# Kernel optimization log

Measured on AMD Instinct MI355X. Metric: run time of the kernel, lower is better.

Reference implementation:

```python
import math
import jax, jax.numpy as jnp
import numpy as np

B, T, E = 1, 4096, 768
H, D = 12, 64
RA_WINDOW = 512
INIT_GATES = (2.2, 0.6, 0.1)


def setup_inputs() -> dict:
    key = jax.random.key(0)
    ks = jax.random.split(key, 6)
    x = jax.random.normal(ks[0], (B, T, E), dtype=jnp.float32)
    # Linear weights stored as [in, out] (math-equivalent to torch's x @ W.T)
    s = 1.0 / math.sqrt(E)
    Wq = jax.random.normal(ks[1], (E, H * D), dtype=jnp.float32) * s
    Wk = jax.random.normal(ks[2], (E, H * D), dtype=jnp.float32) * s
    Wv = jax.random.normal(ks[3], (E, H * D), dtype=jnp.float32) * s
    Wo = jax.random.normal(ks[4], (H * D, E), dtype=jnp.float32) * s
    gates = jnp.tile(jnp.asarray(INIT_GATES, dtype=jnp.float32)[None, :], (H, 1))  # [H,3]
    u = jax.random.normal(ks[5], (H, D), dtype=jnp.float32) * 0.02
    return {"x": x, "Wq": Wq, "Wk": Wk, "Wv": Wv, "Wo": Wo, "gates": gates, "u": u}


def reference(x, Wq, Wk, Wv, Wo, gates, u):
    # projections -> [B,H,T,D]
    def proj(W):
        return (x @ W).reshape(B, T, H, D).transpose(0, 2, 1, 3)
    Q, K, V = proj(Wq), proj(Wk), proj(Wv)

    S = jnp.einsum('bhtd,bhsd->bhts', Q, K) / math.sqrt(D)  # [B,H,T,T]

    w = jax.nn.softmax(gates, axis=-1)  # [H,3]
    w_std = w[:, 0][None, :, None, None]
    w_rec = w[:, 1][None, :, None, None]
    w_disc = w[:, 2][None, :, None, None]

    logits = w_std * S + w_rec * jnp.swapaxes(S, -2, -1)

    # discoverability column bias from K via per-head u
    d_raw = jnp.einsum('bhtd,hd->bht', K, u)
    d = d_raw - jnp.mean(d_raw, axis=-1, keepdims=True)
    logits = logits + w_disc * d[:, :, None, :]

    # causal banded mask
    idx = jnp.arange(T)
    mask = (idx[None, :] <= idx[:, None]) & (jnp.abs(idx[None, :] - idx[:, None]) <= RA_WINDOW)
    logits = jnp.where(mask[None, None, :, :], logits, -jnp.inf)

    attn = jax.nn.softmax(logits, axis=-1)
    ctx = jnp.einsum('bhts,bhsd->bhtd', attn, V)
    out = ctx.transpose(0, 2, 1, 3).reshape(B, T, H * D) @ Wo
    return (out, attn)
```

## Files before the change

### kernel.cpp

```cpp
#include <hip/hip_runtime.h>
#include <cstddef>

#define T_LEN 4096
#define EMB 768
#define NH 12
#define HD 64
#define WIN 512

#define GBM 128
#define GBN 128
#define GBK 16

__global__ __launch_bounds__(256) void gemm3_f32(const float* __restrict__ A,
                                                 const float* __restrict__ B0,
                                                 const float* __restrict__ B1,
                                                 const float* __restrict__ B2,
                                                 float* __restrict__ C0,
                                                 float* __restrict__ C1,
                                                 float* __restrict__ C2,
                                                 int M, int N, int K) {
    __shared__ float As[GBK][GBM + 4];
    __shared__ float Bs[GBK][GBN + 4];
    const int tid = threadIdx.x;
    const int bm = blockIdx.y * GBM;
    const int bn = blockIdx.x * GBN;
    const float* __restrict__ B = (blockIdx.z == 0) ? B0 : (blockIdx.z == 1) ? B1 : B2;
    float* __restrict__ C = (blockIdx.z == 0) ? C0 : (blockIdx.z == 1) ? C1 : C2;

    const int ty = (tid >> 4) << 2;
    const int tx = (tid & 15) << 2;

    const int ar = tid >> 1;
    const int ac = (tid & 1) << 3;
    const int br = tid >> 4;
    const int bc = (tid & 15) << 3;

    float acc[8][8] = {};

    float4 pa0 = *(const float4*)&A[(size_t)(bm + ar) * K + ac];
    float4 pa1 = *(const float4*)&A[(size_t)(bm + ar) * K + ac + 4];
    float4 pb0 = *(const float4*)&B[(size_t)br * N + bn + bc];
    float4 pb1 = *(const float4*)&B[(size_t)br * N + bn + bc + 4];

    for (int k0 = 0; k0 < K; k0 += GBK) {
        As[ac + 0][ar] = pa0.x; As[ac + 1][ar] = pa0.y; As[ac + 2][ar] = pa0.z; As[ac + 3][ar] = pa0.w;
        As[ac + 4][ar] = pa1.x; As[ac + 5][ar] = pa1.y; As[ac + 6][ar] = pa1.z; As[ac + 7][ar] = pa1.w;
        *(float4*)&Bs[br][bc]     = pb0;
        *(float4*)&Bs[br][bc + 4] = pb1;
        __syncthreads();
        if (k0 + GBK < K) {
            pa0 = *(const float4*)&A[(size_t)(bm + ar) * K + k0 + GBK + ac];
            pa1 = *(const float4*)&A[(size_t)(bm + ar) * K + k0 + GBK + ac + 4];
            pb0 = *(const float4*)&B[(size_t)(k0 + GBK + br) * N + bn + bc];
            pb1 = *(const float4*)&B[(size_t)(k0 + GBK + br) * N + bn + bc + 4];
        }
#pragma unroll
        for (int k = 0; k < GBK; ++k) {
            const float4 a0v = *(const float4*)&As[k][ty];
            const float4 a1v = *(const float4*)&As[k][ty + 64];
            const float4 b0v = *(const float4*)&Bs[k][tx];
            const float4 b1v = *(const float4*)&Bs[k][tx + 64];
            const float av[8] = {a0v.x, a0v.y, a0v.z, a0v.w, a1v.x, a1v.y, a1v.z, a1v.w};
            const float bv[8] = {b0v.x, b0v.y, b0v.z, b0v.w, b1v.x, b1v.y, b1v.z, b1v.w};
#pragma unroll
            for (int i = 0; i < 8; ++i)
#pragma unroll
                for (int j = 0; j < 8; ++j)
                    acc[i][j] += av[i] * bv[j];
        }
        __syncthreads();
    }
#pragma unroll
    for (int i = 0; i < 8; ++i) {
        const int r = bm + ty + ((i < 4) ? i : (60 + i));
        *(float4*)&C[(size_t)r * N + bn + tx]      = make_float4(acc[i][0], acc[i][1], acc[i][2], acc[i][3]);
        *(float4*)&C[(size_t)r * N + bn + tx + 64] = make_float4(acc[i][4], acc[i][5], acc[i][6], acc[i][7]);
    }
}

__global__ __launch_bounds__(256) void dbias_kernel(const float* __restrict__ K,
                                                    const float* __restrict__ u,
                                                    float* __restrict__ d_bias) {
    const int h = blockIdx.x;
    const int tid = threadIdx.x;
    __shared__ __align__(16) float us[HD];
    __shared__ float dr[T_LEN];
    __shared__ float red[256];
    if (tid < HD) us[tid] = u[h * HD + tid];
    __syncthreads();
    const float4* u4 = (const float4*)us;
    float lsum = 0.f;
    for (int t = tid; t < T_LEN; t += 256) {
        const float4* Kp = (const float4*)&K[(size_t)t * EMB + h * HD];
        float acc = 0.f;
#pragma unroll
        for (int i = 0; i < HD / 4; ++i) {
            float4 k4 = Kp[i];
            float4 uu = u4[i];
            acc += k4.x * uu.x + k4.y * uu.y + k4.z * uu.z + k4.w * uu.w;
        }
        dr[t] = acc;
        lsum += acc;
    }
    red[tid] = lsum;
    __syncthreads();
    for (int off = 128; off > 0; off >>= 1) {
        if (tid < off) red[tid] += red[tid + off];
        __syncthreads();
    }
    const float mean = red[0] * (1.0f / (float)T_LEN);
    __syncthreads();
    for (int t = tid; t < T_LEN; t += 256) {
        d_bias[h * T_LEN + t] = dr[t] - mean;
    }
}

__global__ __launch_bounds__(256) void attn_band_kernel(const float* __restrict__ Q,
                                                        const float* __restrict__ K,
                                                        const float* __restrict__ V,
                                                        const float* __restrict__ d_bias,
                                                        const float* __restrict__ gates,
                                                        float* __restrict__ attn,
                                                        float* __restrict__ ctx) {
    const int t0  = blockIdx.x << 6;
    const int h   = blockIdx.y;
    const int tid = threadIdx.x;
    const int cg  = tid & 15;
    const int tm  = (tid >> 4) << 2;
    const int tn4 = cg << 2;

    const int lm = tid >> 2;
    const int lk = (tid & 3) << 4;
    const int sr = tid >> 1;
    const int sc = (tid & 1) << 5;

    __shared__ __align__(16) float QT[64][68];
    __shared__ __align__(16) float KT[64][68];
    __shared__ __align__(16) float Bc[64][136];
    __shared__ float cmf[5][64];
    __shared__ float rmf[64], idvf[64];
    float* __restrict__ Bp = &Bc[0][0];

    const float g0 = gates[h * 3 + 0];
    const float g1 = gates[h * 3 + 1];
    const float g2 = gates[h * 3 + 2];
    const float gm = fmaxf(g0, fmaxf(g1, g2));
    const float e0 = __expf(g0 - gm), e1 = __expf(g1 - gm), e2 = __expf(g2 - gm);
    const float gi = 1.0f / (e0 + e1 + e2);
    const float w_std = e0 * gi * 0.125f;
    const float w_rec = e1 * gi * 0.125f;
    const float w_disc = e2 * gi;

    const int cp_start = (t0 >= 576) ? 0 : ((576 - t0) >> 7);
    int s0 = t0 - 576 + (cp_start << 7);

    float4 kr[8], qr[8];
    {
        int srow = s0 + sr; srow = srow < 0 ? 0 : srow;
        const float* Kp = K + (size_t)srow * EMB + h * HD + sc;
#pragma unroll
        for (int c = 0; c < 8; ++c) kr[c] = *(const float4*)(Kp + 4 * c);
    }

    {
        const float* Qp = Q + (size_t)(t0 + lm) * EMB + h * HD + lk;
        const float* Kp = K + (size_t)(t0 + lm) * EMB + h * HD + lk;
#pragma unroll
        for (int it = 0; it < 4; ++it) {
            float4 a = *(const float4*)(Qp + 4 * it);
            QT[lk + 4 * it + 0][lm] = a.x;
            QT[lk + 4 * it + 1][lm] = a.y;
            QT[lk + 4 * it + 2][lm] = a.z;
            QT[lk + 4 * it + 3][lm] = a.w;
            float4 b = *(const float4*)(Kp + 4 * it);
            KT[lk + 4 * it + 0][lm] = b.x;
            KT[lk + 4 * it + 1][lm] = b.y;
            KT[lk + 4 * it + 2][lm] = b.z;
            KT[lk + 4 * it + 3][lm] = b.w;
        }
    }

    float rm[4], rden[4], acc[4][4];
#pragma unroll
    for (int i = 0; i < 4; ++i) {
        rm[i] = -1e30f;
        rden[i] = 0.f;
#pragma unroll
        for (int j = 0; j < 4; ++j) acc[i][j] = 0.f;
    }

    for (int cp = cp_start; cp < 5; ++cp) {
        __syncthreads();
#pragma unroll
        for (int c = 0; c < 8; ++c) {
            Bc[sc + 4 * c + 0][sr] = kr[c].x;
            Bc[sc + 4 * c + 1][sr] = kr[c].y;
            Bc[sc + 4 * c + 2][sr] = kr[c].z;
            Bc[sc + 4 * c + 3][sr] = kr[c].w;
        }
        __syncthreads();

        {
            int srow = s0 + sr; srow = srow < 0 ? 0 : srow;
            const float* Qp = Q + (size_t)srow * EMB + h * HD + sc;
#pragma unroll
            for (int c = 0; c < 8; ++c) qr[c] = *(const float4*)(Qp + 4 * c);
        }

        float m1[4][8] = {};
#pragma unroll 8
        for (int k = 0; k < 64; ++k) {
            const float4 a4 = *(const float4*)&QT[k][tm];
            const float4 b0 = *(const float4*)&Bc[k][tn4];
            const float4 b1 = *(const float4*)&Bc[k][tn4 + 64];
            const float av[4] = {a4.x, a4.y, a4.z, a4.w};
            const float bv[8] = {b0.x, b0.y, b0.z, b0.w, b1.x, b1.y, b1.z, b1.w};
#pragma unroll
            for (int i = 0; i < 4; ++i)
#pragma unroll
                for (int j = 0; j < 8; ++j)
                    m1[i][j] += av[i] * bv[j];
        }
        __syncthreads();

#pragma unroll
        for (int c = 0; c < 8; ++c) {
            Bc[sc + 4 * c + 0][sr] = qr[c].x;
            Bc[sc + 4 * c + 1][sr] = qr[c].y;
            Bc[sc + 4 * c + 2][sr] = qr[c].z;
            Bc[sc + 4 * c + 3][sr] = qr[c].w;
        }
        __syncthreads();

        if (cp < 4) {
            int srow = s0 + 128 + sr; srow = srow < 0 ? 0 : srow;
            const float* Kp = K + (size_t)srow * EMB + h * HD + sc;
#pragma unroll
            for (int c = 0; c < 8; ++c) kr[c] = *(const float4*)(Kp + 4 * c);
        }

        float m2[4][8] = {};
#pragma unroll 8
        for (int k = 0; k < 64; ++k) {
            const float4 a4 = *(const float4*)&KT[k][tm];
            const float4 b0 = *(const float4*)&Bc[k][tn4];
            const float4 b1 = *(const float4*)&Bc[k][tn4 + 64];
            const float av[4] = {a4.x, a4.y, a4.z, a4.w};
            const float bv[8] = {b0.x, b0.y, b0.z, b0.w, b1.x, b1.y, b1.z, b1.w};
#pragma unroll
            for (int i = 0; i < 4; ++i)
#pragma unroll
                for (int j = 0; j < 8; ++j)
                    m2[i][j] += av[i] * bv[j];
        }

        const int i0 = s0 + tn4;
        const int i0c = i0 < 0 ? 0 : i0;
        const float4 db0 = *(const float4*)&d_bias[h * T_LEN + i0c];
        const float4 db1 = *(const float4*)&d_bias[h * T_LEN + s0 + 64 + tn4];
        const float dbv[8] = {db0.x, db0.y, db0.z, db0.w, db1.x, db1.y, db1.z, db1.w};
        float l[4][8];
#pragma unroll
        for (int i = 0; i < 4; ++i) {
            const int t = t0 + tm + i;
#pragma unroll
            for (int j = 0; j < 8; ++j) {
                const int s = s0 + ((j < 4) ? (tn4 + j) : (tn4 + j + 60));
                const float lv = w_std * m1[i][j] + w_rec * m2[i][j] + w_disc * dbv[j];
                const bool valid = (s >= 0) && (s <= t) && (s >= t - WIN);
                l[i][j] = valid ? lv : -1e30f;
            }
        }
#pragma unroll
        for (int i = 0; i < 4; ++i) {
            float cmx = fmaxf(fmaxf(fmaxf(l[i][0], l[i][1]), fmaxf(l[i][2], l[i][3])),
                              fmaxf(fmaxf(l[i][4], l[i][5]), fmaxf(l[i][6], l[i][7])));
#pragma unroll
            for (int off = 1; off < 16; off <<= 1) cmx = fmaxf(cmx, __shfl_xor(cmx, off));
            const float nm = fmaxf(rm[i], cmx);
            const float f = __expf(rm[i] - nm);
            float cs = 0.f;
#pragma unroll
            for (int j = 0; j < 8; ++j) {
                const float p = __expf(l[i][j] - nm);
                l[i][j] = p;
                cs += p;
            }
#pragma unroll
            for (int off = 1; off < 16; off <<= 1) cs += __shfl_xor(cs, off);
            rden[i] = rden[i] * f + cs;
            rm[i] = nm;
#pragma unroll
            for (int j = 0; j < 4; ++j) acc[i][j] *= f;
            if (cg == 0) cmf[cp][tm + i] = nm;
            float* arow = &attn[((size_t)(h * T_LEN + t0 + tm + i)) * T_LEN];
            if (s0 >= 0)
                *(float4*)&arow[s0 + tn4] = make_float4(l[i][0], l[i][1], l[i][2], l[i][3]);
            *(float4*)&arow[s0 + 64 + tn4] = make_float4(l[i][4], l[i][5], l[i][6], l[i][7]);
        }
        __syncthreads();

#pragma unroll
        for (int j = 0; j < 4; ++j) {
            *(float4*)&Bp[(tn4 + j) * 68 + tm] =
                make_float4(l[0][j], l[1][j], l[2][j], l[3][j]);
            *(float4*)&Bp[(tn4 + j + 64) * 68 + tm] =
                make_float4(l[0][j + 4], l[1][j + 4], l[2][j + 4], l[3][j + 4]);
        }
        __syncthreads();

#pragma unroll 8
        for (int k = 0; k < 128; ++k) {
            const float4 av = *(const float4*)&Bp[k * 68 + tm];
            int vrow = s0 + k; vrow = vrow < 0 ? 0 : vrow;
            const float4 bv = *(const float4*)&V[(size_t)vrow * EMB + h * HD + tn4];
            acc[0][0] += av.x * bv.x; acc[0][1] += av.x * bv.y; acc[0][2] += av.x * bv.z; acc[0][3] += av.x * bv.w;
            acc[1][0] += av.y * bv.x; acc[1][1] += av.y * bv.y; acc[1][2] += av.y * bv.z; acc[1][3] += av.y * bv.w;
            acc[2][0] += av.z * bv.x; acc[2][1] += av.z * bv.y; acc[2][2] += av.z * bv.z; acc[2][3] += av.z * bv.w;
            acc[3][0] += av.w * bv.x; acc[3][1] += av.w * bv.y; acc[3][2] += av.w * bv.z; acc[3][3] += av.w * bv.w;
        }
        s0 += 128;
    }

    float idv[4];
#pragma unroll
    for (int i = 0; i < 4; ++i) {
        idv[i] = 1.0f / rden[i];
        *(float4*)&ctx[(size_t)(t0 + tm + i) * EMB + h * HD + tn4] =
            make_float4(acc[i][0] * idv[i], acc[i][1] * idv[i], acc[i][2] * idv[i], acc[i][3] * idv[i]);
    }
    if (cg == 0) {
#pragma unroll
        for (int i = 0; i < 4; ++i) {
            rmf[tm + i] = rm[i];
            idvf[tm + i] = idv[i];
        }
    }
    __syncthreads();
    for (int idx = tid; idx < 320; idx += 256) {
        const int c = idx >> 6, r = idx & 63;
        if (c >= cp_start) cmf[c][r] = __expf(cmf[c][r] - rmf[r]) * idvf[r];
    }
    __syncthreads();
    int ss = t0 - 576 + (cp_start << 7);
    for (int cp = cp_start; cp < 5; ++cp, ss += 128) {
#pragma unroll
        for (int half = 0; half < 2; ++half) {
            const int cbase = ss + (half << 6);
            if (cbase >= 0) {
#pragma unroll
                for (int i = 0; i < 4; ++i) {
                    const float f = cmf[cp][tm + i];
                    float* p = &attn[((size_t)(h * T_LEN + t0 + tm + i)) * T_LEN + cbase + tn4];
                    const float4 v = *(const float4*)p;
                    *(float4*)p = make_float4(v.x * f, v.y * f, v.z * f, v.w * f);
                }
            }
        }
    }
    const int sl = t0 - 576 + (cp_start << 7);
    const int stored_left = sl < 0 ? 0 : sl;
    const int wv = tid >> 6, ln = tid & 63;
    const float4 z4 = make_float4(0.f, 0.f, 0.f, 0.f);
    for (int r = wv; r < 64; r += 4) {
        float* arow = attn + ((size_t)(h * T_LEN + t0 + r)) * T_LEN;
        for (int col = ln << 2; col < stored_left; col += 256)
            *(float4*)&arow[col] = z4;
        for (int col = t0 + 64 + (ln << 2); col < T_LEN; col += 256)
            *(float4*)&arow[col] = z4;
    }
}

extern "C" void kernel_launch(void* const* d_in, const int* in_sizes, int n_in,
                              void* d_out, int out_size, void* d_ws, size_t ws_size,
                              hipStream_t stream) {
    const float* x     = (const float*)d_in[0];
    const float* Wq    = (const float*)d_in[1];
    const float* Wk    = (const float*)d_in[2];
    const float* Wv    = (const float*)d_in[3];
    const float* Wo    = (const float*)d_in[4];
    const float* gates = (const float*)d_in[5];
    const float* u     = (const float*)d_in[6];

    float* out  = (float*)d_out;
    float* attn = out + (size_t)T_LEN * EMB;

    float* ws = (float*)d_ws;
    float* Qb = ws;
    float* Kb = Qb + (size_t)T_LEN * EMB;
    float* Vb = Kb + (size_t)T_LEN * EMB;
    float* Cb = Vb + (size_t)T_LEN * EMB;
    float* Db = Cb + (size_t)T_LEN * EMB;

    gemm3_f32<<<dim3(EMB / GBN, T_LEN / GBM, 3), 256, 0, stream>>>(
        x, Wq, Wk, Wv, Qb, Kb, Vb, T_LEN, EMB, EMB);
    dbias_kernel<<<NH, 256, 0, stream>>>(Kb, u, Db);

    attn_band_kernel<<<dim3(T_LEN / 64, NH), 256, 0, stream>>>(Qb, Kb, Vb, Db, gates,
                                                               attn, Cb);

    gemm3_f32<<<dim3(EMB / GBN, T_LEN / GBM, 1), 256, 0, stream>>>(
        Cb, Wo, Wo, Wo, out, out, out, T_LEN, EMB, EMB);
}
```

Before: 1.496 ms.

## Stage band probabilities in compact buffer and expand attn in separate kernel

The attention kernel now writes unnormalized band probabilities into a compact per-row workspace of 640 columns plus five per-chunk rescale factors, instead of writing into the full attn matrix, re-reading it to rescale, and zero-filling. A new expand kernel writes every attn row once, scaling band values and emitting zeros elsewhere in a single coalesced pass. This removes the read-modify-write over the attn output and the scattered zero stores from the compute kernel. In exchange it adds a large workspace, an extra kernel launch, and an extra write and read of the compact buffer.

After: 1.448 ms. 3.2% less time.

```diff
diff --git a/kernel.cpp b/kernel.cpp
--- a/kernel.cpp
+++ b/kernel.cpp
@@ -6,6 +6,7 @@
 #define NH 12
 #define HD 64
 #define WIN 512
+#define PBW 640
 
 #define GBM 128
 #define GBN 128
@@ -120,7 +121,8 @@
                                                         const float* __restrict__ V,
                                                         const float* __restrict__ d_bias,
                                                         const float* __restrict__ gates,
-                                                        float* __restrict__ attn,
+                                                        float* __restrict__ Pb,
+                                                        float* __restrict__ Fb,
                                                         float* __restrict__ ctx) {
     const int t0  = blockIdx.x << 6;
     const int h   = blockIdx.y;
@@ -293,10 +295,9 @@
 #pragma unroll
             for (int j = 0; j < 4; ++j) acc[i][j] *= f;
             if (cg == 0) cmf[cp][tm + i] = nm;
-            float* arow = &attn[((size_t)(h * T_LEN + t0 + tm + i)) * T_LEN];
-            if (s0 >= 0)
-                *(float4*)&arow[s0 + tn4] = make_float4(l[i][0], l[i][1], l[i][2], l[i][3]);
-            *(float4*)&arow[s0 + 64 + tn4] = make_float4(l[i][4], l[i][5], l[i][6], l[i][7]);
+            float* prow = &Pb[((size_t)(h * T_LEN + t0 + tm + i)) * PBW + (cp << 7)];
+            *(float4*)&prow[tn4]      = make_float4(l[i][0], l[i][1], l[i][2], l[i][3]);
+            *(float4*)&prow[64 + tn4] = make_float4(l[i][4], l[i][5], l[i][6], l[i][7]);
         }
         __syncthreads();
 
@@ -339,35 +340,32 @@
     __syncthreads();
     for (int idx = tid; idx < 320; idx += 256) {
         const int c = idx >> 6, r = idx & 63;
-        if (c >= cp_start) cmf[c][r] = __expf(cmf[c][r] - rmf[r]) * idvf[r];
-    }
-    __syncthreads();
-    int ss = t0 - 576 + (cp_start << 7);
-    for (int cp = cp_start; cp < 5; ++cp, ss += 128) {
-#pragma unroll
-        for (int half = 0; half < 2; ++half) {
-            const int cbase = ss + (half << 6);
-            if (cbase >= 0) {
-#pragma unroll
-                for (int i = 0; i < 4; ++i) {
-                    const float f = cmf[cp][tm + i];
-                    float* p = &attn[((size_t)(h * T_LEN + t0 + tm + i)) * T_LEN + cbase + tn4];
-                    const float4 v = *(const float4*)p;
-                    *(float4*)p = make_float4(v.x * f, v.y * f, v.z * f, v.w * f);
-                }
-            }
-        }
-    }
-    const int sl = t0 - 576 + (cp_start << 7);
-    const int stored_left = sl < 0 ? 0 : sl;
-    const int wv = tid >> 6, ln = tid & 63;
-    const float4 z4 = make_float4(0.f, 0.f, 0.f, 0.f);
-    for (int r = wv; r < 64; r += 4) {
-        float* arow = attn + ((size_t)(h * T_LEN + t0 + r)) * T_LEN;
-        for (int col = ln << 2; col < stored_left; col += 256)
-            *(float4*)&arow[col] = z4;
-        for (int col = t0 + 64 + (ln << 2); col < T_LEN; col += 256)
-            *(float4*)&arow[col] = z4;
+        const float fct = (c >= cp_start) ? __expf(cmf[c][r] - rmf[r]) * idvf[r] : 0.f;
+        Fb[((size_t)(h * T_LEN + t0 + r)) * 5 + c] = fct;
+    }
+}
+
+__global__ __launch_bounds__(256) void attn_expand_kernel(const float* __restrict__ Pb,
+                                                          const float* __restrict__ Fb,
+                                                          float* __restrict__ attn) {
+    const int t = blockIdx.x;
+    const int h = blockIdx.y;
+    const int base = (t & ~63) - 576;
+    const float* prow = Pb + ((size_t)(h * T_LEN + t)) * PBW;
+    const float* frow = Fb + ((size_t)(h * T_LEN + t)) * 5;
+    float f[5];
+#pragma unroll
+    for (int c = 0; c < 5; ++c) f[c] = frow[c];
+    float* arow = attn + ((size_t)(h * T_LEN + t)) * T_LEN;
+    for (int i4 = threadIdx.x << 2; i4 < T_LEN; i4 += 1024) {
+        const int j = i4 - base;
+        float4 v = make_float4(0.f, 0.f, 0.f, 0.f);
+        if (j >= 0 && j < PBW) {
+            const float4 p = *(const float4*)&prow[j];
+            const float ff = f[j >> 7];
+            v = make_float4(p.x * ff, p.y * ff, p.z * ff, p.w * ff);
+        }
+        *(float4*)&arow[i4] = v;
     }
 }
 
@@ -391,13 +389,16 @@
     float* Vb = Kb + (size_t)T_LEN * EMB;
     float* Cb = Vb + (size_t)T_LEN * EMB;
     float* Db = Cb + (size_t)T_LEN * EMB;
+    float* Pb = Db + (size_t)NH * T_LEN;
+    float* Fb = Pb + (size_t)NH * T_LEN * PBW;
 
     gemm3_f32<<<dim3(EMB / GBN, T_LEN / GBM, 3), 256, 0, stream>>>(
         x, Wq, Wk, Wv, Qb, Kb, Vb, T_LEN, EMB, EMB);
     dbias_kernel<<<NH, 256, 0, stream>>>(Kb, u, Db);
 
     attn_band_kernel<<<dim3(T_LEN / 64, NH), 256, 0, stream>>>(Qb, Kb, Vb, Db, gates,
-                                                               attn, Cb);
+                                                               Pb, Fb, Cb);
+    attn_expand_kernel<<<dim3(T_LEN, NH), 256, 0, stream>>>(Pb, Fb, attn);
 
     gemm3_f32<<<dim3(EMB / GBN, T_LEN / GBM, 1), 256, 0, stream>>>(
         Cb, Wo, Wo, Wo, out, out, out, T_LEN, EMB, EMB);
```
